# Kernel tuning notes

Measured on AMD Instinct MI355X. Metric: run time of the kernel, lower is better.

## Reference

```python
import jax, jax.numpy as jnp
import numpy as np

EMB_DIM = 768
NUM_HEADS = 12
OUT_DIM = 768


def setup_inputs() -> dict:
    key = jax.random.key(0)
    k_x, k_q, k_k, k_v, k_o = jax.random.split(key, 5)
    B, N, D = 8, 1024, EMB_DIM
    s = 1.0 / np.sqrt(D)
    return {
        "x": jax.random.normal(k_x, (B, N, D), dtype=jnp.float32),
        # torch nn.Linear weights are stored [out_features, in_features]
        "Wq": jax.random.normal(k_q, (D, D), dtype=jnp.float32) * s,
        "Wk": jax.random.normal(k_k, (D, D), dtype=jnp.float32) * s,
        "Wv": jax.random.normal(k_v, (D, D), dtype=jnp.float32) * s,
        "Wo": jax.random.normal(k_o, (OUT_DIM, D), dtype=jnp.float32) * s,
    }


def _split_heads(t, H):
    # [B, N, D] -> [B*H, N, D//H]  (heads folded into batch, per einsum 'b i d')
    B, N, D = t.shape
    return t.reshape(B, N, H, D // H).transpose(0, 2, 1, 3).reshape(B * H, N, D // H)


def _merge_heads(t, B, H):
    BH, N, dh = t.shape
    return t.reshape(B, H, N, dh).transpose(0, 2, 1, 3).reshape(B, N, H * dh)


def reference(x, Wq, Wk, Wv, Wo):
    B, N, D = x.shape
    H = NUM_HEADS
    dh = D // H
    # q/k/v projections (torch Linear: y = x @ W.T, no bias)
    q = _split_heads(x @ Wq.T, H)
    k = _split_heads(x @ Wk.T, H)
    v = _split_heads(x @ Wv.T, H)
    scale = dh ** (-0.5)
    # dots: 'b i d , b j d -> b i j' -> full [B*H, N, N] score matrix
    dots = jnp.einsum('bid,bjd->bij', q, k) * scale
    attn = jax.nn.softmax(dots, axis=-1)
    # dropout p=0.0 -> identity
    # vect: 'b i d , b d j -> b i j' == attn @ v
    vect = jnp.einsum('bij,bjd->bid', attn, v)
    out = _merge_heads(vect, B, H) @ Wo.T
    return out
```

## Files before the change

kernel.cpp:

```cpp
#include <hip/hip_runtime.h>
#include <hip/hip_bf16.h>
#include <stdint.h>


typedef __bf16 bf16x8 __attribute__((ext_vector_type(8)));
typedef __bf16 bf16x4 __attribute__((ext_vector_type(4)));
typedef float f32x4 __attribute__((ext_vector_type(4)));

#define GAS __attribute__((address_space(1)))
#define LAS __attribute__((address_space(3)))

__device__ __forceinline__ void glds16(const short* gp, short* lp) {
  __builtin_amdgcn_global_load_lds((const GAS void*)gp, (LAS void*)lp, 16, 0, 0);
}

__device__ __forceinline__ float fast_exp2(float x) {
#if __has_builtin(__builtin_amdgcn_exp2f)
  return __builtin_amdgcn_exp2f(x);
#else
  return __expf(x * 0.6931471805599453f);
#endif
}

__device__ __forceinline__ short bfbits(float f) {
  __bf16 b = (__bf16)f;
  union { __bf16 b; short s; } cv; cv.b = b;
  return cv.s;
}

__device__ __forceinline__ void stage8_f32(const float* __restrict__ src, short* dst) {
  float4 f0 = ((const float4*)src)[0];
  float4 f1 = ((const float4*)src)[1];
  bf16x8 t;
  t[0] = (__bf16)f0.x; t[1] = (__bf16)f0.y; t[2] = (__bf16)f0.z; t[3] = (__bf16)f0.w;
  t[4] = (__bf16)f1.x; t[5] = (__bf16)f1.y; t[6] = (__bf16)f1.z; t[7] = (__bf16)f1.w;
  *(bf16x8*)dst = t;
}

__global__ __launch_bounds__(256) void convert_kernel(
    const float* __restrict__ x, const float* __restrict__ Wq,
    const float* __restrict__ Wk, const float* __restrict__ Wv,
    const float* __restrict__ Wo,
    short* __restrict__ xb, short* __restrict__ wqkv, short* __restrict__ wob) {
  int u0 = blockIdx.x * 1024 + threadIdx.x;
#pragma unroll
  for (int i = 0; i < 4; ++i) {
    int u = u0 + i * 256;
    const float* src; short* dst;
    if (u < 786432) { src = x + (size_t)u * 8; dst = xb + (size_t)u * 8; }
    else if (u < 1007616) {
      int r = u - 786432;
      int wsel = r / 73728, off = r % 73728;
      const float* W = (wsel == 0) ? Wq : (wsel == 1) ? Wk : Wv;
      src = W + (size_t)off * 8;
      dst = wqkv + (size_t)r * 8;
    } else {
      int r = u - 1007616;
      src = Wo + (size_t)r * 8; dst = wob + (size_t)r * 8;
    }
    stage8_f32(src, dst);
  }
}

__device__ __forceinline__ void stage_half(const short* __restrict__ g, short* l,
                                           int w, int lane) {
#pragma unroll
  for (int p = 0; p < 2; ++p) {
    int c = (w * 2 + p) * 64 + lane;
    int row = c >> 3;
    int cs = ((c & 7) ^ (row & 7)) * 8;
    glds16(g + (size_t)row * 768 + cs, l + c * 8);
  }
}

__device__ __forceinline__ void stage_b192(const short* __restrict__ g, short* l,
                                           int w, int lane) {
#pragma unroll
  for (int p = 0; p < 3; ++p) {
    int c = (w * 3 + p) * 64 + lane;
    int row = c >> 3;
    int cs = ((c & 7) ^ (row & 7)) * 8;
    glds16(g + (size_t)row * 768 + cs, l + c * 8);
  }
}

__device__ __forceinline__ void bar_fence() {
  asm volatile("" ::: "memory");
  __builtin_amdgcn_s_barrier();
  asm volatile("" ::: "memory");
}

__device__ __forceinline__ void load_a8(const short* base, int wr, int l16, int quad,
                                        bf16x8 (&fa)[4][2]) {
#pragma unroll
  for (int mf = 0; mf < 4; ++mf)
#pragma unroll
    for (int kk = 0; kk < 2; ++kk) {
      int row = wr * 64 + mf * 16 + l16;
      fa[mf][kk] = *(const bf16x8*)&base[row * 64 + ((((kk << 2) + quad) ^ (row & 7)) << 3)];
    }
}

__device__ __forceinline__ void load_b4(const short* base, int rbase, int l16, int quad,
                                        bf16x8 (&fb)[2][2]) {
#pragma unroll
  for (int nf = 0; nf < 2; ++nf)
#pragma unroll
    for (int kk = 0; kk < 2; ++kk) {
      int row = rbase + nf * 16 + l16;
      fb[nf][kk] = *(const bf16x8*)&base[row * 64 + ((((kk << 2) + quad) ^ (row & 7)) << 3)];
    }
}

__device__ __forceinline__ void load_b2(const short* base, int rbase, int l16, int quad,
                                        bf16x8 (&fb)[2]) {
#pragma unroll
  for (int kk = 0; kk < 2; ++kk) {
    int row = rbase + l16;
    fb[kk] = *(const bf16x8*)&base[row * 64 + ((((kk << 2) + quad) ^ (row & 7)) << 3)];
  }
}

__device__ __forceinline__ void mma16(const bf16x8 (&fa)[4][2], const bf16x8 (&fb)[2][2],
                                      f32x4 (&acc)[4][4], int nf0) {
  __builtin_amdgcn_s_setprio(1);
#pragma unroll
  for (int kk = 0; kk < 2; ++kk)
#pragma unroll
    for (int mf = 0; mf < 4; ++mf)
#pragma unroll
      for (int nf = 0; nf < 2; ++nf)
        acc[mf][nf0 + nf] = __builtin_amdgcn_mfma_f32_16x16x32_bf16(
            fa[mf][kk], fb[nf][kk], acc[mf][nf0 + nf], 0, 0, 0);
  __builtin_amdgcn_s_setprio(0);
}

__device__ __forceinline__ void mma16o(const bf16x8 (&fa)[4][2], const bf16x8 (&fb)[2][2],
                                       f32x4 (&acc)[4][3]) {
  __builtin_amdgcn_s_setprio(1);
#pragma unroll
  for (int kk = 0; kk < 2; ++kk)
#pragma unroll
    for (int mf = 0; mf < 4; ++mf)
#pragma unroll
      for (int nf = 0; nf < 2; ++nf)
        acc[mf][nf] = __builtin_amdgcn_mfma_f32_16x16x32_bf16(
            fa[mf][kk], fb[nf][kk], acc[mf][nf], 0, 0, 0);
  __builtin_amdgcn_s_setprio(0);
}

__device__ __forceinline__ void mma8o(const bf16x8 (&fa)[4][2], const bf16x8 (&fb)[2],
                                      f32x4 (&acc)[4][3]) {
  __builtin_amdgcn_s_setprio(1);
#pragma unroll
  for (int kk = 0; kk < 2; ++kk)
#pragma unroll
    for (int mf = 0; mf < 4; ++mf)
      acc[mf][2] = __builtin_amdgcn_mfma_f32_16x16x32_bf16(
          fa[mf][kk], fb[kk], acc[mf][2], 0, 0, 0);
  __builtin_amdgcn_s_setprio(0);
}

__global__ __launch_bounds__(512, 4) void gemm_qkv(
    const short* __restrict__ xb, const short* __restrict__ wqkv,
    short* __restrict__ q, short* __restrict__ k, short* __restrict__ vt) {
  const int lin = blockIdx.x;
  const int xcd = lin & 7, grp = lin >> 3;
  const int by = grp >> 3;
  const int bx = xcd * 8 + (grp & 7);
  const int m0 = bx * 128;
  const int n0g = by * 256;
  const int tid = threadIdx.x;
  const int w = tid >> 6, lane = tid & 63, l16 = lane & 15, quad = lane >> 4;
  const int wr = w >> 2, wc = w & 3;

  __shared__ short sA[8192];
  __shared__ short sB[16384];

  const short* Asrc = xb + (size_t)m0 * 768;
  const short* Bsrc = wqkv + (size_t)n0g * 768;

  f32x4 acc[4][4];
#pragma unroll
  for (int i = 0; i < 4; ++i)
#pragma unroll
    for (int j = 0; j < 4; ++j) acc[i][j] = (f32x4){0.f, 0.f, 0.f, 0.f};

  const int bh = wc >> 1;
  const int rb0 = (wc & 1) * 64;

  for (int t = 0; t < 12; ++t) {
    __syncthreads();
    stage_half(Asrc + (size_t)t * 64, sA, w, lane);
    stage_half(Bsrc + (size_t)t * 64, sB, w, lane);
    stage_half(Bsrc + 98304 + (size_t)t * 64, &sB[8192], w, lane);
    __syncthreads();
    bf16x8 fa[4][2], fb0[2][2], fb1[2][2];
    load_a8(sA, wr, l16, quad, fa);
    load_b4(&sB[bh * 8192], rb0, l16, quad, fb0);
    mma16(fa, fb0, acc, 0);
    load_b4(&sB[bh * 8192], rb0 + 32, l16, quad, fb1);
    mma16(fa, fb1, acc, 2);
  }

  const int wsel = by / 3;
  const int nl0 = (by % 3) * 256 + wc * 64;
  if (wsel == 2) {
#pragma unroll
    for (int mf = 0; mf < 4; ++mf)
#pragma unroll
      for (int nf = 0; nf < 4; ++nf) {
        int token = m0 + wr * 64 + mf * 16 + quad * 4;
        int nl = nl0 + nf * 16 + l16;
        int bhh = (token >> 10) * 12 + (nl >> 6);
        int jt = (token >> 7) & 7;
        int fb = (wr * 2 + (mf >> 1)) * 4 + nf;
        short tmp[4];
#pragma unroll
        for (int r = 0; r < 4; ++r) tmp[r] = bfbits(acc[mf][nf][r]);
        *(uint2*)(vt + (size_t)bhh * 65536 + jt * 8192 + fb * 512 +
                  (l16 + 16 * quad) * 8 + (mf & 1) * 4) = *(const uint2*)tmp;
      }
  } else {
    short* C = wsel ? k : q;
    const float sc = wsel ? 1.0f : 0.1803368801111244f;
#pragma unroll
    for (int mf = 0; mf < 4; ++mf)
#pragma unroll
      for (int nf = 0; nf < 4; ++nf)
#pragma unroll
        for (int r = 0; r < 4; ++r) {
          int row = m0 + wr * 64 + mf * 16 + quad * 4 + r;
          int nl = nl0 + nf * 16 + l16;
          C[(size_t)row * 768 + nl] = bfbits(acc[mf][nf][r] * sc);
        }
  }
}

__device__ __forceinline__ void attn_stage_k(const short* __restrict__ kb, int j0,
                                             short* sK, int w, int lane) {
#pragma unroll
  for (int p = 0; p < 4; ++p) {
    int lin = (w * 4 + p) * 64 + lane;
    int row = lin >> 3;
    int cs = ((lin & 7) ^ (row & 7)) * 8;
    glds16(kb + (size_t)(j0 + row) * 768 + cs, &sK[lin * 8]);
  }
}

__device__ __forceinline__ void attn_stage_v(const short* __restrict__ vb, int jt,
                                             short* sVt, int w, int lane) {
#pragma unroll
  for (int p = 0; p < 4; ++p) {
    int c = (w * 4 + p) * 64 + lane;
    glds16(vb + (size_t)jt * 8192 + (size_t)c * 8, &sVt[c * 8]);
  }
}

__global__ __launch_bounds__(256, 3) void attn_kernel(
    const short* __restrict__ q, const short* __restrict__ k,
    const short* __restrict__ vt, short* __restrict__ vect) {
  const int bh = blockIdx.x % 96;
  const int qt = blockIdx.x / 96;
  const int b = bh / 12, h = bh % 12;
  const int m0 = qt * 128;
  const int tid = threadIdx.x;
  const int w = tid >> 6, lane = tid & 63, l16 = lane & 15, quad = lane >> 4;

  __shared__ short sQ[128 * 64];
  __shared__ short sK[128 * 64];
  __shared__ short sVt[64 * 128];

  const size_t base = (size_t)b * 786432 + (size_t)h * 64;
  const short* kb = k + base;
  const short* vb = vt + (size_t)bh * 65536;

#pragma unroll
  for (int p = 0; p < 4; ++p) {
    int lin = (w * 4 + p) * 64 + lane;
    int row = lin >> 3;
    int cs = ((lin & 7) ^ (row & 7)) * 8;
    glds16(q + base + (size_t)(m0 + row) * 768 + cs, &sQ[lin * 8]);
  }
  attn_stage_k(kb, 0, sK, w, lane);
  attn_stage_v(vb, 0, sVt, w, lane);
  asm volatile("s_waitcnt vmcnt(8)" ::: "memory");
  bar_fence();
  bf16x8 bq[2][2];
#pragma unroll
  for (int g = 0; g < 2; ++g)
#pragma unroll
    for (int kk = 0; kk < 2; ++kk) {
      int row = g * 64 + w * 16 + l16;
      bq[g][kk] = *(const bf16x8*)&sQ[row * 64 + (((kk * 4 + quad) ^ (row & 7)) << 3)];
    }

  f32x4 l4[2];
  l4[0] = (f32x4){0.f, 0.f, 0.f, 0.f};
  l4[1] = (f32x4){0.f, 0.f, 0.f, 0.f};
  f32x4 oacc[2][4];
#pragma unroll
  for (int g = 0; g < 2; ++g)
#pragma unroll
    for (int td = 0; td < 4; ++td) oacc[g][td] = (f32x4){0.f, 0.f, 0.f, 0.f};

  for (int jt = 0; jt < 8; ++jt) {
    asm volatile("s_waitcnt vmcnt(4)" ::: "memory");
    bar_fence();

    bf16x4 pb[2][2][4];
#pragma unroll
    for (int jh = 0; jh < 2; ++jh) {
      f32x4 s[2][4];
#pragma unroll
      for (int g = 0; g < 2; ++g)
#pragma unroll
        for (int ti = 0; ti < 4; ++ti) s[g][ti] = (f32x4){0.f, 0.f, 0.f, 0.f};
      __builtin_amdgcn_s_setprio(1);
#pragma unroll
      for (int kk = 0; kk < 2; ++kk)
#pragma unroll
        for (int ti = 0; ti < 4; ++ti) {
          int row = jh * 64 + ti * 16 + l16;
          bf16x8 a = *(const bf16x8*)&sK[row * 64 + (((kk * 4 + quad) ^ (row & 7)) << 3)];
          s[0][ti] = __builtin_amdgcn_mfma_f32_16x16x32_bf16(a, bq[0][kk], s[0][ti], 0, 0, 0);
          s[1][ti] = __builtin_amdgcn_mfma_f32_16x16x32_bf16(a, bq[1][kk], s[1][ti], 0, 0, 0);
        }
      __builtin_amdgcn_s_setprio(0);
#pragma unroll
      for (int g = 0; g < 2; ++g)
#pragma unroll
        for (int ti = 0; ti < 4; ++ti) {
          f32x4 e;
          e[0] = fast_exp2(s[g][ti][0]);
          e[1] = fast_exp2(s[g][ti][1]);
          e[2] = fast_exp2(s[g][ti][2]);
          e[3] = fast_exp2(s[g][ti][3]);
          l4[g] += e;
          bf16x4 tb;
          tb[0] = (__bf16)e[0]; tb[1] = (__bf16)e[1];
          tb[2] = (__bf16)e[2]; tb[3] = (__bf16)e[3];
          pb[jh][g][ti] = tb;
        }
    }
    asm volatile("s_waitcnt lgkmcnt(0)" ::: "memory");
    __builtin_amdgcn_sched_barrier(0);
    bar_fence();
    if (jt < 7) attn_stage_k(kb, (jt + 1) * 128, sK, w, lane);

    if (jt < 7) { asm volatile("s_waitcnt vmcnt(4)" ::: "memory"); }
    else        { asm volatile("s_waitcnt vmcnt(0)" ::: "memory"); }
    bar_fence();

    __builtin_amdgcn_s_setprio(1);
#pragma unroll
    for (int jh = 0; jh < 2; ++jh)
#pragma unroll
      for (int t2 = 0; t2 < 2; ++t2) {
        union { bf16x4 hh[2]; bf16x8 v; } bp0, bp1;
        bp0.hh[0] = pb[jh][0][2 * t2];
        bp0.hh[1] = pb[jh][0][2 * t2 + 1];
        bp1.hh[0] = pb[jh][1][2 * t2];
        bp1.hh[1] = pb[jh][1][2 * t2 + 1];
        const int fb = (jh * 2 + t2) * 4;
#pragma unroll
        for (int td = 0; td < 4; ++td) {
          bf16x8 av = *(const bf16x8*)&sVt[(fb + td) * 512 + lane * 8];
          oacc[0][td] = __builtin_amdgcn_mfma_f32_16x16x32_bf16(av, bp0.v, oacc[0][td], 0, 0, 0);
          oacc[1][td] = __builtin_amdgcn_mfma_f32_16x16x32_bf16(av, bp1.v, oacc[1][td], 0, 0, 0);
        }
      }
    __builtin_amdgcn_s_setprio(0);
    asm volatile("s_waitcnt lgkmcnt(0)" ::: "memory");
    __builtin_amdgcn_sched_barrier(0);
    bar_fence();
    if (jt < 7) attn_stage_v(vb, jt + 1, sVt, w, lane);
  }

#pragma unroll
  for (int g = 0; g < 2; ++g) {
    float l = (l4[g][0] + l4[g][1]) + (l4[g][2] + l4[g][3]);
    l += __shfl_xor(l, 16);
    l += __shfl_xor(l, 32);
    float inv = 1.0f / l;
    int i_tok = m0 + g * 64 + w * 16 + l16;
#pragma unroll
    for (int td = 0; td < 4; ++td) {
      short tmp[4];
#pragma unroll
      for (int r = 0; r < 4; ++r) tmp[r] = bfbits(oacc[g][td][r] * inv);
      *(uint2*)(vect + base + (size_t)i_tok * 768 + td * 16 + quad * 4) = *(const uint2*)tmp;
    }
  }
}

__global__ __launch_bounds__(512, 2) void gemm_out(
    const short* __restrict__ vect, const short* __restrict__ wob,
    float* __restrict__ out) {
  const int lin = blockIdx.x;
  const int xcd = lin & 7, grp = lin >> 3;
  const int by = grp >> 3;
  const int bx = xcd * 8 + (grp & 7);
  const int m0 = bx * 128;
  const int n0g = by * 192;
  const int tid = threadIdx.x;
  const int w = tid >> 6, lane = tid & 63, l16 = lane & 15, quad = lane >> 4;
  const int wr = w >> 2, wc = w & 3;

  __shared__ short lds[3][20480];

  const short* Asrc = vect + (size_t)m0 * 768;
  const short* Bsrc = wob + (size_t)n0g * 768;

  f32x4 acc[4][3];
#pragma unroll
  for (int i = 0; i < 4; ++i)
#pragma unroll
    for (int j = 0; j < 3; ++j) acc[i][j] = (f32x4){0.f, 0.f, 0.f, 0.f};

  stage_half(Asrc, &lds[0][0], w, lane);
  stage_b192(Bsrc, &lds[0][8192], w, lane);
  stage_half(Asrc + 64, &lds[1][0], w, lane);
  stage_b192(Bsrc + 64, &lds[1][8192], w, lane);
  asm volatile("s_waitcnt vmcnt(5)" ::: "memory");
  bar_fence();

  const int rb0 = wc * 48;
  bf16x8 fa[4][2], fb01[2][2], fb2[2];

#pragma unroll
  for (int t = 0; t < 12; ++t) {
    const int buf = t % 3, nb = (t + 2) % 3;
    const bool pf = (t < 10);
    const short* A = &lds[buf][0];
    const short* Bb = &lds[buf][8192];

    load_a8(A, wr, l16, quad, fa);
    load_b4(Bb, rb0, l16, quad, fb01);
    if (pf) stage_half(Asrc + (size_t)(t + 2) * 64, &lds[nb][0], w, lane);
    bar_fence();
    __builtin_amdgcn_sched_barrier(0);
    mma16o(fa, fb01, acc);
    __builtin_amdgcn_sched_barrier(0);
    bar_fence();

    load_b2(Bb, rb0 + 32, l16, quad, fb2);
    if (pf) {
      stage_b192(Bsrc + (size_t)(t + 2) * 64, &lds[nb][8192], w, lane);
      asm volatile("s_waitcnt vmcnt(5)" ::: "memory");
    } else if (t == 10) {
      asm volatile("s_waitcnt vmcnt(0)" ::: "memory");
    }
    bar_fence();
    __builtin_amdgcn_sched_barrier(0);
    mma8o(fa, fb2, acc);
    __builtin_amdgcn_sched_barrier(0);
    bar_fence();
  }

#pragma unroll
  for (int mf = 0; mf < 4; ++mf)
#pragma unroll
    for (int nf = 0; nf < 3; ++nf)
#pragma unroll
      for (int r = 0; r < 4; ++r) {
        int row = m0 + wr * 64 + mf * 16 + quad * 4 + r;
        int col = n0g + wc * 48 + nf * 16 + l16;
        out[(size_t)row * 768 + col] = acc[mf][nf][r];
      }
}

extern "C" void kernel_launch(void* const* d_in, const int* in_sizes, int n_in,
                              void* d_out, int out_size, void* d_ws, size_t ws_size,
                              hipStream_t stream) {
  const float* x  = (const float*)d_in[0];
  const float* Wq = (const float*)d_in[1];
  const float* Wk = (const float*)d_in[2];
  const float* Wv = (const float*)d_in[3];
  const float* Wo = (const float*)d_in[4];
  float* out = (float*)d_out;

  const size_t MN = (size_t)8192 * 768;
  short* q    = (short*)d_ws;
  short* k    = q + MN;
  short* vt   = k + MN;
  short* vect = q;
  short* wob  = vt + MN;

  short* xb   = (short*)d_out;
  short* wqkv = xb + MN;

  convert_kernel<<<1056, 256, 0, stream>>>(x, Wq, Wk, Wv, Wo, xb, wqkv, wob);
  gemm_qkv<<<576, 512, 0, stream>>>(xb, wqkv, q, k, vt);
  attn_kernel<<<768, 256, 0, stream>>>(q, k, vt, vect);
  gemm_out<<<256, 512, 0, stream>>>(vect, wob, out);
}
```

Before: 172.3 us.

## Shrink gemm_out tile to 64x192 with single-buffered synchronous LDS staging

The output projection GEMM now uses 64-row tiles and 256-thread blocks, launching twice as many blocks. The triple-buffered, prefetch-pipelined LDS schedule with manual waitcnt and barriers is replaced by a plain loop that loads, syncs, then computes. The aim is more blocks in flight, lower LDS use per block and simpler code. The cost is that global loads no longer overlap the MFMA work, and each B tile is reused across fewer rows.

```diff
diff --git a/kernel.cpp b/kernel.cpp
--- a/kernel.cpp
+++ b/kernel.cpp
@@ -73,17 +73,6 @@
   }
 }
 
-__device__ __forceinline__ void stage_b192(const short* __restrict__ g, short* l,
-                                           int w, int lane) {
-#pragma unroll
-  for (int p = 0; p < 3; ++p) {
-    int c = (w * 3 + p) * 64 + lane;
-    int row = c >> 3;
-    int cs = ((c & 7) ^ (row & 7)) * 8;
-    glds16(g + (size_t)row * 768 + cs, l + c * 8);
-  }
-}
-
 __device__ __forceinline__ void bar_fence() {
   asm volatile("" ::: "memory");
   __builtin_amdgcn_s_barrier();
@@ -394,20 +383,20 @@
   }
 }
 
-__global__ __launch_bounds__(512, 2) void gemm_out(
+__global__ __launch_bounds__(256, 2) void gemm_out(
     const short* __restrict__ vect, const short* __restrict__ wob,
     float* __restrict__ out) {
   const int lin = blockIdx.x;
   const int xcd = lin & 7, grp = lin >> 3;
-  const int by = grp >> 3;
-  const int bx = xcd * 8 + (grp & 7);
-  const int m0 = bx * 128;
+  const int by = grp >> 4;
+  const int bx = xcd * 16 + (grp & 15);
+  const int m0 = bx * 64;
   const int n0g = by * 192;
   const int tid = threadIdx.x;
   const int w = tid >> 6, lane = tid & 63, l16 = lane & 15, quad = lane >> 4;
-  const int wr = w >> 2, wc = w & 3;
-
-  __shared__ short lds[3][20480];
+
+  __shared__ short sA[4096];
+  __shared__ short sB[12288];
 
   const short* Asrc = vect + (size_t)m0 * 768;
   const short* Bsrc = wob + (size_t)n0g * 768;
@@ -418,44 +407,31 @@
 #pragma unroll
     for (int j = 0; j < 3; ++j) acc[i][j] = (f32x4){0.f, 0.f, 0.f, 0.f};
 
-  stage_half(Asrc, &lds[0][0], w, lane);
-  stage_b192(Bsrc, &lds[0][8192], w, lane);
-  stage_half(Asrc + 64, &lds[1][0], w, lane);
-  stage_b192(Bsrc + 64, &lds[1][8192], w, lane);
-  asm volatile("s_waitcnt vmcnt(5)" ::: "memory");
-  bar_fence();
-
-  const int rb0 = wc * 48;
-  bf16x8 fa[4][2], fb01[2][2], fb2[2];
-
-#pragma unroll
+  const int rb0 = w * 48;
+
   for (int t = 0; t < 12; ++t) {
-    const int buf = t % 3, nb = (t + 2) % 3;
-    const bool pf = (t < 10);
-    const short* A = &lds[buf][0];
-    const short* Bb = &lds[buf][8192];
-
-    load_a8(A, wr, l16, quad, fa);
-    load_b4(Bb, rb0, l16, quad, fb01);
-    if (pf) stage_half(Asrc + (size_t)(t + 2) * 64, &lds[nb][0], w, lane);
-    bar_fence();
-    __builtin_amdgcn_sched_barrier(0);
+    __syncthreads();
+#pragma unroll
+    for (int p = 0; p < 2; ++p) {
+      int c = p * 256 + tid;
+      int row = c >> 3;
+      int cs = ((c & 7) ^ (row & 7)) * 8;
+      glds16(Asrc + (size_t)t * 64 + (size_t)row * 768 + cs, &sA[c * 8]);
+    }
+#pragma unroll
+    for (int p = 0; p < 6; ++p) {
+      int c = p * 256 + tid;
+      int row = c >> 3;
+      int cs = ((c & 7) ^ (row & 7)) * 8;
+      glds16(Bsrc + (size_t)t * 64 + (size_t)row * 768 + cs, &sB[c * 8]);
+    }
+    __syncthreads();
+    bf16x8 fa[4][2], fb01[2][2], fb2[2];
+    load_a8(sA, 0, l16, quad, fa);
+    load_b4(sB, rb0, l16, quad, fb01);
     mma16o(fa, fb01, acc);
-    __builtin_amdgcn_sched_barrier(0);
-    bar_fence();
-
-    load_b2(Bb, rb0 + 32, l16, quad, fb2);
-    if (pf) {
-      stage_b192(Bsrc + (size_t)(t + 2) * 64, &lds[nb][8192], w, lane);
-      asm volatile("s_waitcnt vmcnt(5)" ::: "memory");
-    } else if (t == 10) {
-      asm volatile("s_waitcnt vmcnt(0)" ::: "memory");
-    }
-    bar_fence();
-    __builtin_amdgcn_sched_barrier(0);
+    load_b2(sB, rb0 + 32, l16, quad, fb2);
     mma8o(fa, fb2, acc);
-    __builtin_amdgcn_sched_barrier(0);
-    bar_fence();
   }
 
 #pragma unroll
@@ -464,8 +440,8 @@
     for (int nf = 0; nf < 3; ++nf)
 #pragma unroll
       for (int r = 0; r < 4; ++r) {
-        int row = m0 + wr * 64 + mf * 16 + quad * 4 + r;
-        int col = n0g + wc * 48 + nf * 16 + l16;
+        int row = m0 + mf * 16 + quad * 4 + r;
+        int col = n0g + w * 48 + nf * 16 + l16;
         out[(size_t)row * 768 + col] = acc[mf][nf][r];
       }
 }
@@ -493,5 +469,5 @@
   convert_kernel<<<1056, 256, 0, stream>>>(x, Wq, Wk, Wv, Wo, xb, wqkv, wob);
   gemm_qkv<<<576, 512, 0, stream>>>(xb, wqkv, q, k, vt);
   attn_kernel<<<768, 256, 0, stream>>>(q, k, vt, vect);
-  gemm_out<<<256, 512, 0, stream>>>(vect, wob, out);
-}
+  gemm_out<<<512, 256, 0, stream>>>(vect, wob, out);
+}
```

Result: no change. 170.6 us (-0.9%).
